# Optimization experiments

Hardware: AMD Instinct MI355X
Metric: run time of the kernel (lower is better)

## Reference

```python
import jax, jax.numpy as jnp
import numpy as np

N = 100000        # nodes
E = 1600000       # edges (avg degree 16)
IN = 128          # in_channels
HID = 256         # hidden_channels
OUT = 2           # out_channels
G = 512           # num graphs in batch


def setup_inputs() -> dict:
    key = jax.random.key(0)
    ks = jax.random.split(key, 10)
    x = jax.random.normal(ks[0], (N, IN), dtype=jnp.float32)
    edge_index = jax.random.randint(ks[1], (2, E), 0, N, dtype=jnp.int64)
    # sorted graph assignment, every graph non-empty (PyG-style batching)
    batch = (jnp.arange(N, dtype=jnp.int64) * G) // N
    s = 1.0 / np.sqrt(IN)
    sh = 1.0 / np.sqrt(2 * HID)
    sh1 = 1.0 / np.sqrt(HID)
    W_l = jax.random.uniform(ks[2], (HID, IN), jnp.float32, -s, s)   # SAGE lin_l (neighbors)
    b_l = jax.random.uniform(ks[3], (HID,), jnp.float32, -s, s)
    W_r = jax.random.uniform(ks[4], (HID, IN), jnp.float32, -s, s)   # SAGE lin_r (root), no bias
    W0 = jax.random.uniform(ks[5], (HID, IN), jnp.float32, -s, s)    # lin0
    b0 = jax.random.uniform(ks[5], (HID,), jnp.float32, -s, s)
    W1 = jax.random.uniform(ks[6], (HID, 2 * HID), jnp.float32, -sh, sh)  # lin1
    b1 = jax.random.uniform(ks[7], (HID,), jnp.float32, -sh, sh)
    W2 = jax.random.uniform(ks[8], (OUT, HID), jnp.float32, -sh1, sh1)    # lin2
    b2 = jax.random.uniform(ks[9], (OUT,), jnp.float32, -sh1, sh1)
    return {"x": x, "edge_index": edge_index, "batch": batch,
            "W_l": W_l, "b_l": b_l, "W_r": W_r,
            "W0": W0, "b0": b0, "W1": W1, "b1": b1, "W2": W2, "b2": b2}


def reference(x, edge_index, batch, W_l, b_l, W_r, W0, b0, W1, b1, W2, b2):
    src, dst = edge_index[0], edge_index[1]
    # SAGEConv: mean-aggregate neighbor features (gather -> scatter-add -> normalize)
    msg_sum = jax.ops.segment_sum(x[src], dst, num_segments=N)          # [N, IN]
    deg = jax.ops.segment_sum(jnp.ones((E,), x.dtype), dst, num_segments=N)
    aggr = msg_sum / jnp.maximum(deg, 1.0)[:, None]
    h = jax.nn.relu(aggr @ W_l.T + b_l + x @ W_r.T)                     # [N, HID]
    # global max pool per graph
    hp = jax.ops.segment_max(h, batch, num_segments=G)                  # [G, HID]
    # root node = first node of each graph (batch is sorted)
    root = jnp.searchsorted(batch, jnp.arange(G, dtype=batch.dtype))    # [G]
    news = jax.nn.relu(x[root] @ W0.T + b0)                             # [G, HID]
    h = jax.nn.relu(jnp.concatenate([news, hp], axis=-1) @ W1.T + b1)   # [G, HID]
    h = h @ W2.T + b2                                                   # [G, OUT]
    return jax.nn.log_softmax(h, axis=-1)
```

## Files before the change

kernel.cpp:

```cpp
#include <hip/hip_runtime.h>
#include <hip/hip_bf16.h>
#include <math.h>
#include <stdint.h>

#define IN_C 128
#define HID  256
#define OUT_C 2

#define BSHIFT 9
#define BNODES 512
#define EPB 4096

typedef __attribute__((ext_vector_type(8))) short short8;
typedef __attribute__((ext_vector_type(4))) float f32x4;
typedef __attribute__((ext_vector_type(2))) float f32x2;

#if defined(__has_builtin)
#if __has_builtin(__builtin_amdgcn_cvt_pk_f32_fp8) && __has_builtin(__builtin_amdgcn_cvt_pk_fp8_f32)
#define HAVE_FP8_CVT 1
#endif
#endif

__device__ __forceinline__ ushort f2bf(float f) {
  uint32_t u = __float_as_uint(f);
  uint32_t r = u + 0x7FFF + ((u >> 16) & 1);
  return (ushort)(r >> 16);
}
__device__ __forceinline__ float bf2f(ushort b) {
  return __uint_as_float(((uint32_t)b) << 16);
}

#ifndef HAVE_FP8_CVT
__device__ __forceinline__ uint32_t f2fp8_1(float f) {
  uint32_t u = __float_as_uint(f);
  uint32_t s = (u >> 24) & 0x80;
  float a = fabsf(f);
  if (a >= 448.f) return s | 0x7E;
  if (a < 0.015625f) {
    uint32_t m = (uint32_t)(a * 512.f + 0.5f);
    return s | m;
  }
  uint32_t r = u & 0x7fffffff;
  r += 0x7FFFF + ((r >> 20) & 1);
  uint32_t e = (r >> 23) - 127;
  if ((int)e > 8) return s | 0x7E;
  return s | ((e + 7) << 3) | ((r >> 20) & 7);
}
__device__ __forceinline__ float fp8_2f(uint32_t b) {
  uint32_t s = (b & 0x80) << 24;
  uint32_t e = (b >> 3) & 0xF, m = b & 7;
  if (e == 0) { float f = (float)m * 0.001953125f; return s ? -f : f; }
  return __uint_as_float(s | ((e + 120) << 23) | (m << 20));
}
#endif

__device__ __forceinline__ void acc8f8(float* s, uint2 v) {
#ifdef HAVE_FP8_CVT
  f32x2 a = __builtin_amdgcn_cvt_pk_f32_fp8(v.x, false);
  f32x2 b = __builtin_amdgcn_cvt_pk_f32_fp8(v.x, true);
  f32x2 c = __builtin_amdgcn_cvt_pk_f32_fp8(v.y, false);
  f32x2 d = __builtin_amdgcn_cvt_pk_f32_fp8(v.y, true);
  s[0] += a.x; s[1] += a.y; s[2] += b.x; s[3] += b.y;
  s[4] += c.x; s[5] += c.y; s[6] += d.x; s[7] += d.y;
#else
  s[0] += fp8_2f(v.x & 0xff);        s[1] += fp8_2f((v.x >> 8) & 0xff);
  s[2] += fp8_2f((v.x >> 16) & 0xff); s[3] += fp8_2f(v.x >> 24);
  s[4] += fp8_2f(v.y & 0xff);        s[5] += fp8_2f((v.y >> 8) & 0xff);
  s[6] += fp8_2f((v.y >> 16) & 0xff); s[7] += fp8_2f(v.y >> 24);
#endif
}


__global__ void k_hist(const int* __restrict__ dst, int* __restrict__ bcount, int E) {
  __shared__ int h[256];
  int t = threadIdx.x;
  h[t] = 0;
  __syncthreads();
  for (int e = blockIdx.x * 256 + t; e < E; e += gridDim.x * 256)
    atomicAdd(&h[dst[e] >> BSHIFT], 1);
  __syncthreads();
  if (h[t]) atomicAdd(&bcount[t], h[t]);
}

__global__ void k_bucket_scan(const int* __restrict__ bcount,
                              int* __restrict__ bbase, int* __restrict__ bcursor) {
  __shared__ int sd[256];
  int t = threadIdx.x;
  int cnt = bcount[t];
  sd[t] = cnt;
  __syncthreads();
  for (int off = 1; off < 256; off <<= 1) {
    int v = (t >= off) ? sd[t - off] : 0;
    __syncthreads();
    sd[t] += v;
    __syncthreads();
  }
  int base = sd[t] - cnt;
  bbase[t] = base;
  bcursor[t] = base;
}

__global__ __launch_bounds__(256) void k_scatter(
    const int* __restrict__ src, const int* __restrict__ dst,
    int* __restrict__ bcursor, uint32_t* __restrict__ rec, int E) {
  __shared__ int h[256];
  __shared__ int bbase[256];
  __shared__ int lcur[256];
  int t = threadIdx.x;
  int e0 = blockIdx.x * EPB;
  int e1 = e0 + EPB < E ? e0 + EPB : E;
  h[t] = 0; lcur[t] = 0;
  __syncthreads();
  for (int e = e0 + t; e < e1; e += 256)
    atomicAdd(&h[dst[e] >> BSHIFT], 1);
  __syncthreads();
  if (h[t]) bbase[t] = atomicAdd(&bcursor[t], h[t]);
  __syncthreads();
  for (int e = e0 + t; e < e1; e += 256) {
    int d = dst[e];
    int b = d >> BSHIFT;
    int r = atomicAdd(&lcur[b], 1);
    rec[bbase[b] + r] = ((uint32_t)src[e] << BSHIFT) | ((uint32_t)d & (BNODES - 1));
  }
}

__global__ __launch_bounds__(256) void k_csr(
    const uint32_t* __restrict__ rec, const int* __restrict__ bbase,
    const int* __restrict__ bcount,
    int* __restrict__ row_start, int* __restrict__ deg,
    int* __restrict__ csr, int n) {
  __shared__ int ldeg[BNODES];
  __shared__ int lexcl[BNODES];
  __shared__ int ssum[256];
  int t = threadIdx.x;
  int b = blockIdx.x;
  int node0 = b << BSHIFT;
  int ebase = bbase[b];
  int ecnt = bcount[b];

  ldeg[t] = 0; ldeg[t + 256] = 0;
  __syncthreads();
  for (int i = t; i < ecnt; i += 256)
    atomicAdd(&ldeg[rec[ebase + i] & (BNODES - 1)], 1);
  __syncthreads();

  int v0 = ldeg[2 * t], v1 = ldeg[2 * t + 1];
  ssum[t] = v0 + v1;
  __syncthreads();
  for (int off = 1; off < 256; off <<= 1) {
    int v = (t >= off) ? ssum[t - off] : 0;
    __syncthreads();
    ssum[t] += v;
    __syncthreads();
  }
  int excl = ssum[t] - (v0 + v1);
  lexcl[2 * t] = excl;
  lexcl[2 * t + 1] = excl + v0;
  int node = node0 + 2 * t;
  if (node < n) { row_start[node] = ebase + excl; deg[node] = v0; }
  if (node + 1 < n) { row_start[node + 1] = ebase + excl + v0; deg[node + 1] = v1; }
  ldeg[2 * t] = 0; ldeg[2 * t + 1] = 0;
  __syncthreads();
  for (int i = t; i < ecnt; i += 256) {
    uint32_t r = rec[ebase + i];
    int li = r & (BNODES - 1);
    int k = atomicAdd(&ldeg[li], 1);
    csr[ebase + lexcl[li] + k] = (int)(r >> BSHIFT);
  }
}


__global__ void k_cast(const float* __restrict__ in, ushort* __restrict__ outb,
                       uint32_t* __restrict__ outf8, int n4) {
  int i = blockIdx.x * 256 + threadIdx.x;
  if (i < n4) {
    float4 v = ((const float4*)in)[i];
    ushort4 o;
    o.x = f2bf(v.x); o.y = f2bf(v.y); o.z = f2bf(v.z); o.w = f2bf(v.w);
    ((ushort4*)outb)[i] = o;
#ifdef HAVE_FP8_CVT
    int p = __builtin_amdgcn_cvt_pk_fp8_f32(v.x, v.y, 0, false);
    p = __builtin_amdgcn_cvt_pk_fp8_f32(v.z, v.w, p, true);
    outf8[i] = (uint32_t)p;
#else
    outf8[i] = f2fp8_1(v.x) | (f2fp8_1(v.y) << 8) | (f2fp8_1(v.z) << 16) |
               (f2fp8_1(v.w) << 24);
#endif
  }
}

__global__ void k_wcat(const float* __restrict__ Wl, const float* __restrict__ Wr,
                       ushort* __restrict__ Wcat) {
  int c = blockIdx.x, k = threadIdx.x;
  float v = (k < IN_C) ? Wl[(size_t)c * IN_C + k] : Wr[(size_t)c * IN_C + (k - IN_C)];
  Wcat[(size_t)c * (2 * IN_C) + k] = f2bf(v);
}


__global__ void k_aggr(const uint32_t* __restrict__ xf8, const int* __restrict__ csr,
                       const int* __restrict__ row_start, const int* __restrict__ deg,
                       ushort* __restrict__ aggr, int n) {
  int wid = threadIdx.x >> 6;
  int lane = threadIdx.x & 63;
  int node = blockIdx.x * 4 + wid;
  if (node >= n) return;
  int base = row_start[node];
  int d = deg[node];
  int q = lane >> 4, li = lane & 15;
  float s[8] = {};
  int i = q;
  for (; i + 12 < d; i += 16) {
    int n0 = csr[base + i];
    int n1 = csr[base + i + 4];
    int n2 = csr[base + i + 8];
    int n3 = csr[base + i + 12];
    uint2 a = ((const uint2*)(xf8 + (size_t)n0 * (IN_C / 4)))[li];
    uint2 b = ((const uint2*)(xf8 + (size_t)n1 * (IN_C / 4)))[li];
    uint2 c = ((const uint2*)(xf8 + (size_t)n2 * (IN_C / 4)))[li];
    uint2 e = ((const uint2*)(xf8 + (size_t)n3 * (IN_C / 4)))[li];
    acc8f8(s, a); acc8f8(s, b); acc8f8(s, c); acc8f8(s, e);
  }
  for (; i < d; i += 4) {
    int n0 = csr[base + i];
    uint2 a = ((const uint2*)(xf8 + (size_t)n0 * (IN_C / 4)))[li];
    acc8f8(s, a);
  }
#pragma unroll
  for (int j = 0; j < 8; ++j) {
    s[j] += __shfl_xor(s[j], 16);
    s[j] += __shfl_xor(s[j], 32);
  }
  if (q == 0) {
    float inv = 1.0f / (float)(d > 1 ? d : 1);
    uint4 o;
    o.x = (uint32_t)f2bf(s[0] * inv) | ((uint32_t)f2bf(s[1] * inv) << 16);
    o.y = (uint32_t)f2bf(s[2] * inv) | ((uint32_t)f2bf(s[3] * inv) << 16);
    o.z = (uint32_t)f2bf(s[4] * inv) | ((uint32_t)f2bf(s[5] * inv) << 16);
    o.w = (uint32_t)f2bf(s[6] * inv) | ((uint32_t)f2bf(s[7] * inv) << 16);
    ((uint4*)(aggr + (size_t)node * IN_C))[li] = o;
  }
}


__global__ __launch_bounds__(256, 2) void k_gemm_pool(
    const ushort* __restrict__ aggrb, const ushort* __restrict__ xb,
    const ushort* __restrict__ Wcat, const float* __restrict__ bl,
    const int* __restrict__ batch, float* __restrict__ hp, int n) {
  __shared__ ushort sA[128][40];
  __shared__ ushort sB[256][40];
  __shared__ float sbl[256];
  __shared__ int sBatch[128];

  int t = threadIdx.x;
  int n0 = blockIdx.x * 128;
  sbl[t] = bl[t];
  if (t < 128) sBatch[t] = (n0 + t < n) ? batch[n0 + t] : -1;

  int lane = t & 63, w = t >> 6;
  int q = lane >> 4, m = lane & 15;

  f32x4 acc[8][4] = {};

  for (int k0 = 0; k0 < 2 * IN_C; k0 += 32) {
    __syncthreads();
#pragma unroll
    for (int it = 0; it < 2; ++it) {
      int j = it * 256 + t;
      int r = j >> 2, kA = (j & 3) * 8;
      int gn = n0 + r; gn = gn < n ? gn : n - 1;
      const ushort* srcA = (k0 < IN_C) ? (aggrb + (size_t)gn * IN_C + k0 + kA)
                                       : (xb + (size_t)gn * IN_C + (k0 - IN_C) + kA);
      *(uint4*)&sA[r][kA] = *(const uint4*)srcA;
    }
#pragma unroll
    for (int it = 0; it < 4; ++it) {
      int j = it * 256 + t;
      int c = j >> 2, kB = (j & 3) * 8;
      *(uint4*)&sB[c][kB] = *(const uint4*)(Wcat + (size_t)c * (2 * IN_C) + k0 + kB);
    }
    __syncthreads();

    short8 af[8], bf[4];
#pragma unroll
    for (int rt = 0; rt < 8; ++rt) af[rt] = *(const short8*)&sA[rt * 16 + m][q * 8];
#pragma unroll
    for (int ct = 0; ct < 4; ++ct) bf[ct] = *(const short8*)&sB[w * 64 + ct * 16 + m][q * 8];
#pragma unroll
    for (int rt = 0; rt < 8; ++rt)
#pragma unroll
      for (int ct = 0; ct < 4; ++ct)
        acc[rt][ct] = __builtin_amdgcn_mfma_f32_16x16x32_bf16(af[rt], bf[ct], acc[rt][ct], 0, 0, 0);
  }

  int last = n - 1 - n0; last = last < 127 ? last : 127;
  int gA = sBatch[0];
  int gB = sBatch[last];
#pragma unroll
  for (int ct = 0; ct < 4; ++ct) {
    int col = w * 64 + ct * 16 + m;
    float bias = sbl[col];
    float mA = 0.f, mB = 0.f;
#pragma unroll
    for (int rt = 0; rt < 8; ++rt) {
#pragma unroll
      for (int i = 0; i < 4; ++i) {
        int lr = rt * 16 + q * 4 + i;
        if (n0 + lr < n) {
          float v = fmaxf(acc[rt][ct][i] + bias, 0.f);
          if (sBatch[lr] == gA) mA = fmaxf(mA, v);
          else mB = fmaxf(mB, v);
        }
      }
    }
    mA = fmaxf(mA, __shfl_xor(mA, 16)); mA = fmaxf(mA, __shfl_xor(mA, 32));
    mB = fmaxf(mB, __shfl_xor(mB, 16)); mB = fmaxf(mB, __shfl_xor(mB, 32));
    if (q == 0) {
      atomicMax((int*)&hp[(size_t)gA * HID + col], __float_as_int(mA));
      if (gB != gA) atomicMax((int*)&hp[(size_t)gB * HID + col], __float_as_int(mB));
    }
  }
}


__global__ void k_root(const int* __restrict__ batch, int* __restrict__ root, int n) {
  int i = blockIdx.x * 256 + threadIdx.x;
  if (i < n) {
    int g = batch[i];
    if (i == 0 || batch[i - 1] != g) root[g] = i;
  }
}


__global__ __launch_bounds__(256) void k_mlp2(
    const float* __restrict__ x, const float* __restrict__ hp,
    const int* __restrict__ root,
    const float* __restrict__ W0, const float* __restrict__ b0,
    const float* __restrict__ W1, const float* __restrict__ b1,
    const float* __restrict__ W2, const float* __restrict__ b2,
    float* __restrict__ out) {
  __shared__ float xr[IN_C];
  __shared__ float cat[2 * HID];
  __shared__ float h2r[HID];
  __shared__ float red[8];

  int g = blockIdx.x;
  int t = threadIdx.x;
  int rg = root[g];
  if (t < IN_C) xr[t] = x[(size_t)rg * IN_C + t];
  __syncthreads();

  float a0 = b0[t];
  const float* w0 = W0 + (size_t)t * IN_C;
#pragma unroll 4
  for (int k = 0; k < IN_C; ++k) a0 += xr[k] * w0[k];
  cat[t] = fmaxf(a0, 0.f);
  cat[HID + t] = hp[(size_t)g * HID + t];
  __syncthreads();

  float a1 = b1[t];
  const float* w1 = W1 + (size_t)t * (2 * HID);
#pragma unroll 4
  for (int j = 0; j < 2 * HID; ++j) a1 += cat[j] * w1[j];
  h2r[t] = fmaxf(a1, 0.f);
  __syncthreads();

  float p0 = h2r[t] * W2[t];
  float p1 = h2r[t] * W2[HID + t];
  for (int off = 32; off > 0; off >>= 1) {
    p0 += __shfl_down(p0, off);
    p1 += __shfl_down(p1, off);
  }
  int lane = t & 63, wid = t >> 6;
  if (lane == 0) { red[wid * 2] = p0; red[wid * 2 + 1] = p1; }
  __syncthreads();
  if (t == 0) {
    float l0 = b2[0] + red[0] + red[2] + red[4] + red[6];
    float l1 = b2[1] + red[1] + red[3] + red[5] + red[7];
    float mx = fmaxf(l0, l1);
    float ls = logf(expf(l0 - mx) + expf(l1 - mx));
    out[(size_t)g * 2 + 0] = l0 - mx - ls;
    out[(size_t)g * 2 + 1] = l1 - mx - ls;
  }
}


extern "C" void kernel_launch(void* const* d_in, const int* in_sizes, int n_in,
                              void* d_out, int out_size, void* d_ws, size_t ws_size,
                              hipStream_t stream) {
  const float* x  = (const float*)d_in[0];
  const int* ei   = (const int*)d_in[1];
  const int* batch= (const int*)d_in[2];
  const float* Wl = (const float*)d_in[3];
  const float* bl = (const float*)d_in[4];
  const float* Wr = (const float*)d_in[5];
  const float* W0 = (const float*)d_in[6];
  const float* b0 = (const float*)d_in[7];
  const float* W1 = (const float*)d_in[8];
  const float* b1 = (const float*)d_in[9];
  const float* W2 = (const float*)d_in[10];
  const float* b2 = (const float*)d_in[11];
  float* out = (float*)d_out;

  const int N = in_sizes[0] / IN_C;
  const int E = in_sizes[1] / 2;
  const int G = out_size / OUT_C;
  const int* src = ei;
  const int* dst = ei + E;
  const int NB = (N + BNODES - 1) >> BSHIFT;

  char* w = (char*)d_ws;
  int* deg       = (int*)w; w += (size_t)N * 4;
  int* row_start = (int*)w; w += (size_t)N * 4;
  int* bcount    = (int*)w; w += 1024;
  int* bbase     = (int*)w; w += 1024;
  int* bcursor   = (int*)w; w += 1024;
  int* root      = (int*)w; w += (size_t)G * 4;
  w = (char*)(((uintptr_t)w + 255) & ~(uintptr_t)255);
  int* csr       = (int*)w; w += (size_t)E * 4;
  w = (char*)(((uintptr_t)w + 255) & ~(uintptr_t)255);
  ushort* xb     = (ushort*)w; w += (size_t)N * IN_C * 2;
  uint32_t* xf8  = (uint32_t*)w; w += (size_t)N * IN_C;
  ushort* aggrb  = (ushort*)w; w += (size_t)N * IN_C * 2;
  ushort* Wcat   = (ushort*)w; w += (size_t)HID * (2 * IN_C) * 2;
  float* hp      = (float*)w; w += (size_t)G * HID * 4;
  uint32_t* rec  = (uint32_t*)aggrb;

  hipMemsetAsync(bcount, 0, 1024, stream);
  hipMemsetAsync(hp, 0, (size_t)G * HID * 4, stream);

  k_cast<<<((N * IN_C / 4) + 255) / 256, 256, 0, stream>>>(x, xb, xf8, N * IN_C / 4);
  k_wcat<<<HID, 2 * IN_C, 0, stream>>>(Wl, Wr, Wcat);
  k_hist<<<1024, 256, 0, stream>>>(dst, bcount, E);
  k_bucket_scan<<<1, 256, 0, stream>>>(bcount, bbase, bcursor);
  k_scatter<<<(E + EPB - 1) / EPB, 256, 0, stream>>>(src, dst, bcursor, rec, E);
  k_csr<<<NB, 256, 0, stream>>>(rec, bbase, bcount, row_start, deg, csr, N);
  k_root<<<(N + 255) / 256, 256, 0, stream>>>(batch, root, N);
  k_aggr<<<(N + 3) / 4, 256, 0, stream>>>(xf8, csr, row_start, deg, aggrb, N);
  k_gemm_pool<<<(N + 127) / 128, 256, 0, stream>>>(aggrb, xb, Wcat, bl, batch, hp, N);
  k_mlp2<<<G, 256, 0, stream>>>(x, hp, root, W0, b0, W1, b1, W2, b2, out);
}
```

Baseline: 331.5 us.

## Double-buffer GEMM-pool tiles via direct global-to-LDS loads with XOR swizzle

Rewrites the fused SAGE GEMM + max-pool kernel to use 64-row tiles, double-buffered LDS staged through global_load_lds, and an XOR-swizzled unpadded LDS layout. The aim is to overlap the next K-slice loads with the current MFMAs, remove the register round trip on loads, and avoid LDS bank conflicts. The smaller tile doubles the block count and raises the share of re-reading the weight matrix per row. It also drops the two-blocks-per-SM launch bound.

After: 331.3 us. Within noise of the previous version (-0.1%).

```diff
diff --git a/kernel.cpp b/kernel.cpp
--- a/kernel.cpp
+++ b/kernel.cpp
@@ -18,6 +18,9 @@
 #if defined(__has_builtin)
 #if __has_builtin(__builtin_amdgcn_cvt_pk_f32_fp8) && __has_builtin(__builtin_amdgcn_cvt_pk_fp8_f32)
 #define HAVE_FP8_CVT 1
+#endif
+#if __has_builtin(__builtin_amdgcn_global_load_lds)
+#define HAVE_GLL 1
 #endif
 #endif
 
@@ -242,57 +245,108 @@
 }
 
 
-__global__ __launch_bounds__(256, 2) void k_gemm_pool(
+#ifdef HAVE_GLL
+__device__ __forceinline__ void load16_lds(const ushort* g, ushort* l) {
+  __builtin_amdgcn_global_load_lds(
+      (const __attribute__((address_space(1))) uint32_t*)g,
+      (__attribute__((address_space(3))) uint32_t*)l, 16, 0, 0);
+}
+#endif
+
+__global__ __launch_bounds__(256) void k_gemm_pool(
     const ushort* __restrict__ aggrb, const ushort* __restrict__ xb,
     const ushort* __restrict__ Wcat, const float* __restrict__ bl,
     const int* __restrict__ batch, float* __restrict__ hp, int n) {
-  __shared__ ushort sA[128][40];
-  __shared__ ushort sB[256][40];
+  __shared__ ushort sA[2][64 * 32];
+  __shared__ ushort sB[2][256 * 32];
   __shared__ float sbl[256];
-  __shared__ int sBatch[128];
-
-  int t = threadIdx.x;
-  int n0 = blockIdx.x * 128;
+  __shared__ int sBatch[64];
+
+  int t = threadIdx.x;
+  int n0 = blockIdx.x * 64;
   sbl[t] = bl[t];
-  if (t < 128) sBatch[t] = (n0 + t < n) ? batch[n0 + t] : -1;
+  if (t < 64) sBatch[t] = (n0 + t < n) ? batch[n0 + t] : -1;
 
   int lane = t & 63, w = t >> 6;
   int q = lane >> 4, m = lane & 15;
 
-  f32x4 acc[8][4] = {};
-
-  for (int k0 = 0; k0 < 2 * IN_C; k0 += 32) {
-    __syncthreads();
-#pragma unroll
-    for (int it = 0; it < 2; ++it) {
-      int j = it * 256 + t;
-      int r = j >> 2, kA = (j & 3) * 8;
-      int gn = n0 + r; gn = gn < n ? gn : n - 1;
-      const ushort* srcA = (k0 < IN_C) ? (aggrb + (size_t)gn * IN_C + k0 + kA)
-                                       : (xb + (size_t)gn * IN_C + (k0 - IN_C) + kA);
-      *(uint4*)&sA[r][kA] = *(const uint4*)srcA;
+  int rA = t >> 2, pA = t & 3;
+  int cA = pA ^ ((rA >> 1) & 3);
+  int gnA = n0 + rA; gnA = gnA < n ? gnA : n - 1;
+  const ushort* baseAggr = aggrb + (size_t)gnA * IN_C + cA * 8;
+  const ushort* baseX    = xb + (size_t)gnA * IN_C + cA * 8;
+  int ldsA = rA * 32 + pA * 8;
+  int pchunk = q ^ ((m >> 1) & 3);
+
+  f32x4 acc[4][4] = {};
+
+#ifdef HAVE_GLL
+  auto stage = [&](int k0, int buf) {
+    const ushort* srcA = (k0 < 4) ? baseAggr + k0 * 32 : baseX + (k0 - 4) * 32;
+    load16_lds(srcA, &sA[buf][ldsA]);
+#pragma unroll
+    for (int it = 0; it < 4; ++it) {
+      int rB = it * 64 + (t >> 2);
+      int cB = (t & 3) ^ ((rB >> 1) & 3);
+      load16_lds(Wcat + (size_t)rB * (2 * IN_C) + k0 * 32 + cB * 8,
+                 &sB[buf][rB * 32 + (t & 3) * 8]);
     }
-#pragma unroll
-    for (int it = 0; it < 4; ++it) {
-      int j = it * 256 + t;
-      int c = j >> 2, kB = (j & 3) * 8;
-      *(uint4*)&sB[c][kB] = *(const uint4*)(Wcat + (size_t)c * (2 * IN_C) + k0 + kB);
-    }
-    __syncthreads();
-
-    short8 af[8], bf[4];
-#pragma unroll
-    for (int rt = 0; rt < 8; ++rt) af[rt] = *(const short8*)&sA[rt * 16 + m][q * 8];
-#pragma unroll
-    for (int ct = 0; ct < 4; ++ct) bf[ct] = *(const short8*)&sB[w * 64 + ct * 16 + m][q * 8];
-#pragma unroll
-    for (int rt = 0; rt < 8; ++rt)
+  };
+  stage(0, 0);
+  __syncthreads();
+#pragma unroll
+  for (int k0 = 0; k0 < 8; ++k0) {
+    int cur = k0 & 1;
+    if (k0 < 7) stage(k0 + 1, cur ^ 1);
+    short8 af[4], bf[4];
+#pragma unroll
+    for (int rt = 0; rt < 4; ++rt)
+      af[rt] = *(const short8*)&sA[cur][(rt * 16 + m) * 32 + pchunk * 8];
+#pragma unroll
+    for (int ct = 0; ct < 4; ++ct)
+      bf[ct] = *(const short8*)&sB[cur][(w * 64 + ct * 16 + m) * 32 + pchunk * 8];
+#pragma unroll
+    for (int rt = 0; rt < 4; ++rt)
 #pragma unroll
       for (int ct = 0; ct < 4; ++ct)
         acc[rt][ct] = __builtin_amdgcn_mfma_f32_16x16x32_bf16(af[rt], bf[ct], acc[rt][ct], 0, 0, 0);
-  }
-
-  int last = n - 1 - n0; last = last < 127 ? last : 127;
+    __syncthreads();
+  }
+#else
+  for (int k0 = 0; k0 < 8; ++k0) {
+    const ushort* srcA = (k0 < 4) ? baseAggr + k0 * 32 : baseX + (k0 - 4) * 32;
+    uint4 vA = *(const uint4*)srcA;
+    uint4 vB[4];
+#pragma unroll
+    for (int it = 0; it < 4; ++it) {
+      int rB = it * 64 + (t >> 2);
+      int cB = (t & 3) ^ ((rB >> 1) & 3);
+      vB[it] = *(const uint4*)(Wcat + (size_t)rB * (2 * IN_C) + k0 * 32 + cB * 8);
+    }
+    __syncthreads();
+    *(uint4*)&sA[0][ldsA] = vA;
+#pragma unroll
+    for (int it = 0; it < 4; ++it) {
+      int rB = it * 64 + (t >> 2);
+      *(uint4*)&sB[0][rB * 32 + (t & 3) * 8] = vB[it];
+    }
+    __syncthreads();
+    short8 af[4], bf[4];
+#pragma unroll
+    for (int rt = 0; rt < 4; ++rt)
+      af[rt] = *(const short8*)&sA[0][(rt * 16 + m) * 32 + pchunk * 8];
+#pragma unroll
+    for (int ct = 0; ct < 4; ++ct)
+      bf[ct] = *(const short8*)&sB[0][(w * 64 + ct * 16 + m) * 32 + pchunk * 8];
+#pragma unroll
+    for (int rt = 0; rt < 4; ++rt)
+#pragma unroll
+      for (int ct = 0; ct < 4; ++ct)
+        acc[rt][ct] = __builtin_amdgcn_mfma_f32_16x16x32_bf16(af[rt], bf[ct], acc[rt][ct], 0, 0, 0);
+  }
+#endif
+
+  int last = n - 1 - n0; last = last < 63 ? last : 63;
   int gA = sBatch[0];
   int gB = sBatch[last];
 #pragma unroll
@@ -301,7 +355,7 @@
     float bias = sbl[col];
     float mA = 0.f, mB = 0.f;
 #pragma unroll
-    for (int rt = 0; rt < 8; ++rt) {
+    for (int rt = 0; rt < 4; ++rt) {
 #pragma unroll
       for (int i = 0; i < 4; ++i) {
         int lr = rt * 16 + q * 4 + i;
@@ -436,6 +490,6 @@
   k_csr<<<NB, 256, 0, stream>>>(rec, bbase, bcount, row_start, deg, csr, N);
   k_root<<<(N + 255) / 256, 256, 0, stream>>>(batch, root, N);
   k_aggr<<<(N + 3) / 4, 256, 0, stream>>>(xf8, csr, row_start, deg, aggrb, N);
-  k_gemm_pool<<<(N + 127) / 128, 256, 0, stream>>>(aggrb, xb, Wcat, bl, batch, hp, N);
+  k_gemm_pool<<<(N + 63) / 64, 256, 0, stream>>>(aggrb, xb, Wcat, bl, batch, hp, N);
   k_mlp2<<<G, 256, 0, stream>>>(x, hp, root, W0, b0, W1, b1, W2, b2, out);
 }
```
